# Performance work log

Measured on AMD Instinct MI355X. Metric: run time of the kernel, lower is better.

Reference implementation:

```python
import jax, jax.numpy as jnp
import numpy as np

EPS = 1e-8
SCALE = 23.0
LEAKY_SLOPE = 0.01  # torch nn.LeakyReLU default

M, B, D = 65536, 2048, 13
H1, H2, H3 = 300, 600, 100


def _linear_params(key, out_f, in_f):
    # torch nn.Linear default init: U(-1/sqrt(in), 1/sqrt(in))
    k1, k2 = jax.random.split(key)
    bound = 1.0 / np.sqrt(in_f)
    W = jax.random.uniform(k1, (out_f, in_f), jnp.float32, -bound, bound)
    b = jax.random.uniform(k2, (out_f,), jnp.float32, -bound, bound)
    return W, b


def setup_inputs() -> dict:
    key = jax.random.key(0)
    ks = jax.random.split(key, 6)
    memory = jax.random.normal(ks[0], (M, D), jnp.float32)
    value = jax.random.normal(ks[1], (B, D), jnp.float32)
    W1, b1 = _linear_params(ks[2], H1, D)
    W2, b2 = _linear_params(ks[3], H2, H1)
    W3, b3 = _linear_params(ks[4], H3, H2)
    W4, b4 = _linear_params(ks[5], D, H3)
    return {"memory": memory, "value": value,
            "W1": W1, "b1": b1, "W2": W2, "b2": b2,
            "W3": W3, "b3": b3, "W4": W4, "b4": b4}


def _mlp(x, W1, b1, W2, b2, W3, b3, W4, b4):
    h = jax.nn.relu(x @ W1.T + b1)                      # [M, 300]
    h = jax.nn.leaky_relu(h @ W2.T + b2, LEAKY_SLOPE)   # [M, 600]
    h = jax.nn.relu(h @ W3.T + b3)                      # [M, 100]
    return jax.nn.leaky_relu(h @ W4.T + b4, LEAKY_SLOPE)  # [M, 13]


def reference(memory, value, W1, b1, W2, b2, W3, b3, W4, b4):
    # abstract_memory = self.net(self.memory)
    t1 = _mlp(memory, W1, b1, W2, b2, W3, b3, W4, b4)   # [M, 13]
    t2 = value.reshape(value.shape[0], -1)              # flatten(value, 1) -> [B, 13]
    # cosine similarity with torch eps clamping on each norm
    t1n = t1 / jnp.maximum(jnp.linalg.norm(t1, axis=-1, keepdims=True), EPS)
    t2n = t2 / jnp.maximum(jnp.linalg.norm(t2, axis=-1, keepdims=True), EPS)
    s = (t2n @ t1n.T) * SCALE                           # [B, M], replaces per-row python loop
    return jnp.max(s, axis=1)                           # [B]
```

## Files before the change

### kernel.cpp

```cpp
#include <hip/hip_runtime.h>


typedef __bf16 bf16x8 __attribute__((ext_vector_type(8)));
typedef float f32x16 __attribute__((ext_vector_type(16)));

constexpr size_t OFF_W1B = 0;
constexpr size_t OFF_W2B = 10240;
constexpr size_t OFF_W3B = 419840;
constexpr size_t OFF_W4B = 583680;
constexpr size_t OFF_T2N = 591872;
constexpr size_t OFF_T1N = 657408;
constexpr size_t OFF_PART= 2754560;

__device__ __forceinline__ bf16x8 ld8(const __bf16* p) {
    return *reinterpret_cast<const bf16x8*>(p);
}
__device__ __forceinline__ f32x16 mfma32(bf16x8 a, bf16x8 b, f32x16 c) {
    return __builtin_amdgcn_mfma_f32_32x32x16_bf16(a, b, c, 0, 0, 0);
}

__device__ __forceinline__ void cvtswap(const f32x16& a, bf16x8& f0, bf16x8& f1) {
    unsigned w[8];
    #pragma unroll
    for (int j = 0; j < 8; j++)
        asm("v_cvt_pk_bf16_f32 %0, %1, %2" : "=v"(w[j]) : "v"(a[2*j]), "v"(a[2*j+1]));
    unsigned a0 = w[0], b0 = w[2]; asm("v_permlane32_swap_b32 %0, %1" : "+v"(a0), "+v"(b0));
    unsigned a1 = w[1], b1 = w[3]; asm("v_permlane32_swap_b32 %0, %1" : "+v"(a1), "+v"(b1));
    unsigned a2 = w[4], b2 = w[6]; asm("v_permlane32_swap_b32 %0, %1" : "+v"(a2), "+v"(b2));
    unsigned a3 = w[5], b3 = w[7]; asm("v_permlane32_swap_b32 %0, %1" : "+v"(a3), "+v"(b3));
    union { unsigned u[4]; bf16x8 v; } p, q;
    p.u[0] = a0; p.u[1] = a1; p.u[2] = b0; p.u[3] = b1; f0 = p.v;
    q.u[0] = a2; q.u[1] = a3; q.u[2] = b2; q.u[3] = b3; f1 = q.v;
}

__global__ void prep_kernel(const float* __restrict__ W1, const float* __restrict__ b1,
                            const float* __restrict__ W2, const float* __restrict__ b2,
                            const float* __restrict__ W3, const float* __restrict__ b3,
                            const float* __restrict__ W4, const float* __restrict__ b4,
                            const float* __restrict__ value, char* __restrict__ ws) {
    __bf16* W1B = (__bf16*)(ws + OFF_W1B);
    __bf16* W2B = (__bf16*)(ws + OFF_W2B);
    __bf16* W3B = (__bf16*)(ws + OFF_W3B);
    __bf16* W4B = (__bf16*)(ws + OFF_W4B);
    __bf16* T2N = (__bf16*)(ws + OFF_T2N);

    int idx = blockIdx.x * 256 + threadIdx.x;
    if (idx < 5120) {
        int e = idx & 7, lane = (idx >> 3) & 63, nt = idx >> 9;
        int n = nt*32 + (lane & 31);
        int k = (lane >> 5)*8 + e;
        float v = 0.0f;
        if (n < 300)       v = (k < 13) ? W1[n*13 + k] : (k == 13 ? b1[n] : 0.0f);
        else if (n == 300) v = (k == 13) ? 1.0f : 0.0f;
        W1B[idx] = (__bf16)v;
        return;
    }
    idx -= 5120;
    if (idx < 204800) {
        int e = idx & 7, lane = (idx >> 3) & 63, r = idx >> 9;
        int ks = r % 20, nt = r / 20;
        int n = nt*32 + (lane & 31);
        int k = ks*16 + (lane >> 5)*8 + e;
        float v = 0.0f;
        if (n < 600)       v = (k < 300) ? W2[n*300 + k] : (k == 300 ? b2[n] : 0.0f);
        else if (n == 600) v = (k == 300) ? 1.0f : 0.0f;
        W2B[idx] = (__bf16)v;
        return;
    }
    idx -= 204800;
    if (idx < 81920) {
        int e = idx & 7, lane = (idx >> 3) & 63, r = idx >> 9;
        int ks = r % 40, nt = r / 40;
        int n = nt*32 + (lane & 31);
        int k = ks*16 + (lane >> 5)*8 + e;
        float v = 0.0f;
        if (n < 100)       v = (k < 600) ? W3[n*600 + k] : (k == 600 ? b3[n] : 0.0f);
        else if (n == 100) v = (k == 600) ? 1.0f : 0.0f;
        W3B[idx] = (__bf16)v;
        return;
    }
    idx -= 81920;
    if (idx < 4096) {
        int e = idx & 7, lane = (idx >> 3) & 63, ks = idx >> 9;
        int n = lane & 31;
        int k = ks*16 + (lane >> 5)*8 + e;
        float v = 0.0f;
        if (n < 13) v = (k < 100) ? W4[n*100 + k] : (k == 100 ? b4[n] : 0.0f);
        W4B[idx] = (__bf16)v;
        return;
    }
    idx -= 4096;
    if (idx < 2048) {
        float v[13]; float s = 0.0f;
        #pragma unroll
        for (int k = 0; k < 13; k++) { v[k] = value[idx*13 + k]; s += v[k]*v[k]; }
        float inv = 1.0f / fmaxf(sqrtf(s), 1e-8f);
        #pragma unroll
        for (int k = 0; k < 13; k++) T2N[idx*16 + k] = (__bf16)(v[k] * inv);
        #pragma unroll
        for (int k = 13; k < 16; k++) T2N[idx*16 + k] = (__bf16)0.0f;
    }
}

__global__ __launch_bounds__(256, 2) void mlp_kernel(const float* __restrict__ mem,
                                                     char* __restrict__ ws) {
    __shared__ char smem[47616];
    __bf16* stg = (__bf16*)smem;
    float*  t1s = (float*)(smem + 40960);

    const __bf16* W1B = (const __bf16*)(ws + OFF_W1B);
    const __bf16* W2B = (const __bf16*)(ws + OFF_W2B);
    const __bf16* W3B = (const __bf16*)(ws + OFF_W3B);
    const __bf16* W4B = (const __bf16*)(ws + OFF_W4B);
    __bf16* T1N = (__bf16*)(ws + OFF_T1N);

    const int tid = threadIdx.x;
    const int wave = tid >> 6, lane = tid & 63;
    const int l31 = lane & 31, hi = lane >> 5;
    const int bm0 = blockIdx.x * 128;
    const int m = bm0 + wave*32 + l31;

    bf16x8 sreg[5];
    #pragma unroll
    for (int i = 0; i < 5; i++)
        sreg[i] = ld8(W2B + (size_t)(tid + i*256)*8);

    bf16x8 xf;
    {
        union { __bf16 h[8]; bf16x8 v; } u;
        const float* xr = mem + (size_t)m*13;
        if (hi == 0) {
            #pragma unroll
            for (int e = 0; e < 8; e++) u.h[e] = (__bf16)xr[e];
        } else {
            #pragma unroll
            for (int e = 0; e < 5; e++) u.h[e] = (__bf16)xr[8 + e];
            u.h[5] = (__bf16)1.0f;
            u.h[6] = (__bf16)0.0f;
            u.h[7] = (__bf16)0.0f;
        }
        xf = u.v;
    }

    bf16x8 afc[20];
    #pragma unroll
    for (int nt = 0; nt < 10; nt++) {
        bf16x8 wf = ld8(W1B + (size_t)nt*512 + lane*8);
        f32x16 z = {};
        f32x16 a = mfma32(wf, xf, z);
        #pragma unroll
        for (int r = 0; r < 16; r++) a[r] = fmaxf(a[r], 0.0f);
        cvtswap(a, afc[2*nt], afc[2*nt + 1]);
    }

    #pragma unroll
    for (int i = 0; i < 5; i++)
        *reinterpret_cast<bf16x8*>(stg + (tid + i*256)*8) = sreg[i];
    __syncthreads();

    f32x16 acc3[4] = {};
    int buf = 0;
    for (int nt2 = 0; nt2 < 20; nt2++) {
        if (nt2 < 19) {
            #pragma unroll
            for (int i = 0; i < 5; i++)
                sreg[i] = ld8(W2B + (size_t)(nt2 + 1)*10240 + (size_t)(tid + i*256)*8);
        }
        const __bf16* sb = stg + buf*10240;
        f32x16 e0 = {}, e1 = {};
        #pragma unroll
        for (int ks = 0; ks < 20; ks += 2) {
            e0 = mfma32(ld8(sb + ks*512 + lane*8),       afc[ks],     e0);
            e1 = mfma32(ld8(sb + (ks + 1)*512 + lane*8), afc[ks + 1], e1);
        }
        #pragma unroll
        for (int r = 0; r < 16; r++) {
            float v = e0[r] + e1[r];
            e0[r] = fmaxf(v, 0.0f) + 0.01f*fminf(v, 0.0f);
        }
        bf16x8 h2f0, h2f1;
        cvtswap(e0, h2f0, h2f1);
        #pragma unroll
        for (int n3 = 0; n3 < 4; n3++) {
            const __bf16* bp = W3B + ((size_t)(n3*40 + 2*nt2)*64 + lane)*8;
            acc3[n3] = mfma32(ld8(bp),       h2f0, acc3[n3]);
            acc3[n3] = mfma32(ld8(bp + 512), h2f1, acc3[n3]);
        }
        if (nt2 < 19) {
            #pragma unroll
            for (int i = 0; i < 5; i++)
                *reinterpret_cast<bf16x8*>(stg + (buf^1)*10240 + (tid + i*256)*8) = sreg[i];
        }
        __syncthreads();
        buf ^= 1;
    }

    f32x16 acc4 = {};
    #pragma unroll
    for (int n3 = 0; n3 < 4; n3++) {
        f32x16 h;
        #pragma unroll
        for (int r = 0; r < 16; r++) h[r] = fmaxf(acc3[n3][r], 0.0f);
        bf16x8 f0, f1;
        cvtswap(h, f0, f1);
        acc4 = mfma32(ld8(W4B + (size_t)(2*n3)*512 + lane*8),     f0, acc4);
        acc4 = mfma32(ld8(W4B + (size_t)(2*n3 + 1)*512 + lane*8), f1, acc4);
    }
    const int mrow = wave*32 + l31;
    #pragma unroll
    for (int r = 0; r < 16; r++) {
        const int n4 = (r & 3) + 8*(r >> 2) + 4*hi;
        if (n4 < 13) {
            float v = acc4[r];
            t1s[mrow*13 + n4] = fmaxf(v, 0.0f) + 0.01f*fminf(v, 0.0f);
        }
    }
    __syncthreads();

    if (tid < 128) {
        float s = 0.0f, v[13];
        #pragma unroll
        for (int k = 0; k < 13; k++) { v[k] = t1s[tid*13 + k]; s += v[k]*v[k]; }
        const float inv = 1.0f / fmaxf(sqrtf(s), 1e-8f);
        union { __bf16 o[16]; bf16x8 f[2]; } u;
        #pragma unroll
        for (int k = 0; k < 13; k++) u.o[k] = (__bf16)(v[k] * inv);
        #pragma unroll
        for (int k = 13; k < 16; k++) u.o[k] = (__bf16)0.0f;
        bf16x8* dst = reinterpret_cast<bf16x8*>(T1N + (size_t)(bm0 + tid)*16);
        dst[0] = u.f[0];
        dst[1] = u.f[1];
    }
}

__global__ __launch_bounds__(256) void sim_kernel(const char* __restrict__ ws_c,
                                                  float* __restrict__ part) {
    const char* ws = ws_c;
    const __bf16* T1N = (const __bf16*)(ws + OFF_T1N);
    const __bf16* T2N = (const __bf16*)(ws + OFF_T2N);
    const int wave = threadIdx.x >> 6, lane = threadIdx.x & 63;
    const int l31 = lane & 31, hi = lane >> 5;
    const int bgroup = blockIdx.x & 15, ms = blockIdx.x >> 4;
    const int b0 = (bgroup*4 + wave) * 32;

    const bf16x8 af = ld8(T2N + (size_t)(b0 + l31)*16 + hi*8);
    const f32x16 zero = {};
    f32x16 mx;
    #pragma unroll
    for (int r = 0; r < 16; r++) mx[r] = -3.0e38f;

    #pragma unroll 4
    for (int mt = ms; mt < 2048; mt += 128) {
        bf16x8 bf0 = ld8(T1N + ((size_t)mt*32 + l31)*16 + hi*8);
        bf16x8 bf1 = ld8(T1N + ((size_t)(mt + 64)*32 + l31)*16 + hi*8);
        f32x16 d0 = mfma32(af, bf0, zero);
        f32x16 d1 = mfma32(af, bf1, zero);
        #pragma unroll
        for (int r = 0; r < 16; r++)
            mx[r] = fmaxf(mx[r], fmaxf(d0[r], d1[r]));
    }
    #pragma unroll
    for (int off = 1; off <= 16; off <<= 1) {
        #pragma unroll
        for (int r = 0; r < 16; r++) mx[r] = fmaxf(mx[r], __shfl_xor(mx[r], off));
    }
    if (l31 == 0) {
        #pragma unroll
        for (int reg = 0; reg < 16; reg++)
            part[ms*2048 + b0 + (reg & 3) + 8*(reg >> 2) + 4*hi] = mx[reg];
    }
}

__global__ void reduce_kernel(const float* __restrict__ part, float* __restrict__ out) {
    int b = blockIdx.x*256 + threadIdx.x;
    if (b < 2048) {
        float m = part[b];
        #pragma unroll
        for (int ms = 1; ms < 64; ms++) m = fmaxf(m, part[ms*2048 + b]);
        out[b] = 23.0f * m;
    }
}

extern "C" void kernel_launch(void* const* d_in, const int* in_sizes, int n_in,
                              void* d_out, int out_size, void* d_ws, size_t ws_size,
                              hipStream_t stream) {
    const float* memory = (const float*)d_in[0];
    const float* value  = (const float*)d_in[1];
    const float* W1 = (const float*)d_in[2]; const float* b1 = (const float*)d_in[3];
    const float* W2 = (const float*)d_in[4]; const float* b2 = (const float*)d_in[5];
    const float* W3 = (const float*)d_in[6]; const float* b3 = (const float*)d_in[7];
    const float* W4 = (const float*)d_in[8]; const float* b4 = (const float*)d_in[9];
    char* ws = (char*)d_ws;
    float* part = (float*)(ws + OFF_PART);
    float* out = (float*)d_out;

    prep_kernel<<<1164, 256, 0, stream>>>(W1, b1, W2, b2, W3, b3, W4, b4, value, ws);
    mlp_kernel<<<512, 256, 0, stream>>>(memory, ws);
    sim_kernel<<<1024, 256, 0, stream>>>(ws, part);
    reduce_kernel<<<8, 256, 0, stream>>>(part, out);
}
```

Before: 124.9 us.

## Read W2 fragments directly from global memory instead of LDS double buffering

Removes the LDS double-buffered staging of W2 tiles along with the per-iteration __syncthreads. Each wave now loads its W2 fragments straight from global memory (L1/L2 cached), and the W3 fragment loads are hoisted to the top of each iteration. This cuts LDS usage and block-wide barriers, which could raise occupancy and reduce sync stalls. In exchange, every wave issues its own global/L2 traffic for the shared W2 weights, so cache bandwidth may become the limit.

```diff
diff --git a/kernel.cpp b/kernel.cpp
--- a/kernel.cpp
+++ b/kernel.cpp
@@ -104,9 +104,7 @@
 
 __global__ __launch_bounds__(256, 2) void mlp_kernel(const float* __restrict__ mem,
                                                      char* __restrict__ ws) {
-    __shared__ char smem[47616];
-    __bf16* stg = (__bf16*)smem;
-    float*  t1s = (float*)(smem + 40960);
+    __shared__ float t1s[128*13];
 
     const __bf16* W1B = (const __bf16*)(ws + OFF_W1B);
     const __bf16* W2B = (const __bf16*)(ws + OFF_W2B);
@@ -119,11 +117,6 @@
     const int l31 = lane & 31, hi = lane >> 5;
     const int bm0 = blockIdx.x * 128;
     const int m = bm0 + wave*32 + l31;
-
-    bf16x8 sreg[5];
-    #pragma unroll
-    for (int i = 0; i < 5; i++)
-        sreg[i] = ld8(W2B + (size_t)(tid + i*256)*8);
 
     bf16x8 xf;
     {
@@ -153,25 +146,21 @@
         cvtswap(a, afc[2*nt], afc[2*nt + 1]);
     }
 
-    #pragma unroll
-    for (int i = 0; i < 5; i++)
-        *reinterpret_cast<bf16x8*>(stg + (tid + i*256)*8) = sreg[i];
-    __syncthreads();
-
     f32x16 acc3[4] = {};
-    int buf = 0;
     for (int nt2 = 0; nt2 < 20; nt2++) {
-        if (nt2 < 19) {
-            #pragma unroll
-            for (int i = 0; i < 5; i++)
-                sreg[i] = ld8(W2B + (size_t)(nt2 + 1)*10240 + (size_t)(tid + i*256)*8);
-        }
-        const __bf16* sb = stg + buf*10240;
+        bf16x8 wf3[8];
+        #pragma unroll
+        for (int n3 = 0; n3 < 4; n3++) {
+            const __bf16* bp3 = W3B + ((size_t)(n3*40 + 2*nt2)*64 + lane)*8;
+            wf3[2*n3]     = ld8(bp3);
+            wf3[2*n3 + 1] = ld8(bp3 + 512);
+        }
+        const __bf16* bp2 = W2B + (size_t)nt2*10240 + lane*8;
         f32x16 e0 = {}, e1 = {};
         #pragma unroll
         for (int ks = 0; ks < 20; ks += 2) {
-            e0 = mfma32(ld8(sb + ks*512 + lane*8),       afc[ks],     e0);
-            e1 = mfma32(ld8(sb + (ks + 1)*512 + lane*8), afc[ks + 1], e1);
+            e0 = mfma32(ld8(bp2 + ks*512),       afc[ks],     e0);
+            e1 = mfma32(ld8(bp2 + (ks + 1)*512), afc[ks + 1], e1);
         }
         #pragma unroll
         for (int r = 0; r < 16; r++) {
@@ -182,17 +171,9 @@
         cvtswap(e0, h2f0, h2f1);
         #pragma unroll
         for (int n3 = 0; n3 < 4; n3++) {
-            const __bf16* bp = W3B + ((size_t)(n3*40 + 2*nt2)*64 + lane)*8;
-            acc3[n3] = mfma32(ld8(bp),       h2f0, acc3[n3]);
-            acc3[n3] = mfma32(ld8(bp + 512), h2f1, acc3[n3]);
-        }
-        if (nt2 < 19) {
-            #pragma unroll
-            for (int i = 0; i < 5; i++)
-                *reinterpret_cast<bf16x8*>(stg + (buf^1)*10240 + (tid + i*256)*8) = sreg[i];
-        }
-        __syncthreads();
-        buf ^= 1;
+            acc3[n3] = mfma32(wf3[2*n3],     h2f0, acc3[n3]);
+            acc3[n3] = mfma32(wf3[2*n3 + 1], h2f1, acc3[n3]);
+        }
     }
 
     f32x16 acc4 = {};
```

After: 137.2 us. 1.1x slower.
